# Kernel tuning notes

Measured on AMD Instinct MI355X. Metric: run time of the kernel, lower is better.

## Reference

```python
import math
import jax, jax.numpy as jnp
import numpy as np

COLORS = 10
MAX_SHIFT = 5
B, H, W = 32, 128, 128

_shifts = [(dy, dx) for dy in range(-MAX_SHIFT, MAX_SHIFT + 1)
           for dx in range(-MAX_SHIFT, MAX_SHIFT + 1)
           if not (dy == 0 and dx == 0)]  # include_identity=False
DYS = jnp.asarray(np.array([s[0] for s in _shifts], dtype=np.int32))
DXS = jnp.asarray(np.array([s[1] for s in _shifts], dtype=np.int32))


def _shift_all(grid):
    """Apply every (dy,dx) shift to an int grid [B,H,W] with zero padding.

    out[s, b, y, x] = grid[b, y-dy_s, x-dx_s] if in-bounds else 0,
    exactly matching apply_shift_batch (uncovered regions are color 0).
    Returns [S, B, H, W].
    """
    b, h, w = grid.shape
    padded = jnp.pad(grid, ((0, 0), (MAX_SHIFT, MAX_SHIFT), (MAX_SHIFT, MAX_SHIFT)))
    def one(dy, dx):
        return jax.lax.dynamic_slice(padded, (0, MAX_SHIFT - dy, MAX_SHIFT - dx), (b, h, w))
    return jax.vmap(one)(DYS, DXS)


def setup_inputs() -> dict:
    key = jax.random.key(0)
    k1, k2, k3 = jax.random.split(key, 3)
    return {
        "demo_in": jax.random.randint(k1, (B, H, W), 0, COLORS, dtype=jnp.int32),
        "demo_out": jax.random.randint(k2, (B, H, W), 0, COLORS, dtype=jnp.int32),
        "query_in": jax.random.randint(k3, (B, H, W), 0, COLORS, dtype=jnp.int32),
        "color_log_weight": jnp.zeros((COLORS,), dtype=jnp.float32),
        "logit_scale": jnp.asarray(4.0, dtype=jnp.float32),
    }


def reference(demo_in, demo_out, query_in, color_log_weight, logit_scale):
    b, h, w = query_in.shape
    S = DYS.shape[0]

    # Per-shift correlation score. one_hot(shifted)*one_hot(demo_out)*w summed
    # over (C,H,W) == sum over pixels of w[demo_out] * (shifted == demo_out).
    shifted_demo = _shift_all(demo_in)                       # [S,B,H,W] int
    w_out = jnp.exp(color_log_weight)[demo_out]              # [B,H,W]
    eq = (shifted_demo == demo_out[None]).astype(jnp.float32)
    match = jnp.sum(eq * w_out[None], axis=(2, 3))           # [S,B]
    scale = jnp.minimum(jnp.exp(logit_scale), 100.0)
    scores = match.T / math.sqrt(h * w) * scale              # [B,S]
    attention = jax.nn.softmax(scores, axis=1)               # [B,S]

    # Weighted accumulation of one-hot shifted queries, done as a scatter-add
    # into the color channel (avoids materializing [S,B,C,H,W]).
    shifted_query = _shift_all(query_in)                     # [S,B,H,W] int
    b_idx = jnp.arange(b)[None, :, None, None]
    y_idx = jnp.arange(h)[None, None, :, None]
    x_idx = jnp.arange(w)[None, None, None, :]
    attn_b = jnp.broadcast_to(attention.T[:, :, None, None], (S, b, h, w))
    accum = jnp.zeros((b, COLORS, h, w), dtype=jnp.float32)
    accum = accum.at[b_idx, shifted_query, y_idx, x_idx].add(attn_b)
    return jnp.log(jnp.maximum(accum, 1e-6))
```

## Files before the change

### kernel.cpp

```cpp
#include <hip/hip_runtime.h>
#include <hip/hip_bf16.h>
#include <math.h>

#define COLORS 10
#define NB 32
#define H 128
#define W 128
#define NS 120
#define HW (H*W)
#define STRIPS 8
#define SH 16
#define DROWS 26
#define DINW 8

typedef unsigned char u8;
typedef unsigned int u32;
typedef unsigned long long u64;
typedef float f32x4 __attribute__((ext_vector_type(4)));
typedef short bf16x8 __attribute__((ext_vector_type(8)));

__global__ __launch_bounds__(512) void match_strip(
    const int* __restrict__ demo_in, const int* __restrict__ demo_out,
    const float* __restrict__ clw, float* __restrict__ mpart)
{
    __shared__ u32 din_p[COLORS][DROWS][DINW];
    __shared__ u32 dout_p[COLORS][SH][4];
    __shared__ float wexp[COLORS];

    int t = threadIdx.x;
    int strip = blockIdx.x;
    int b = blockIdx.y;
    int wave = t >> 6, lane = t & 63;

    if (t < COLORS) wexp[t] = __expf(clw[t]);

    const int* di = demo_in  + b * HW;
    const int* dd = demo_out + b * HW;
    int y0 = strip * SH;

    for (int r = wave; r < DROWS; r += 8) {
        int gy = y0 - 5 + r;
        bool ok = (gy >= 0 && gy < H);
        int v0 = 0, v1 = 0;
        if (ok) { v0 = di[gy * W + lane]; v1 = di[gy * W + 64 + lane]; }
        #pragma unroll
        for (int c = 0; c < COLORS; c++) {
            u64 h0 = __ballot(v0 == c);
            u64 h1 = __ballot(v1 == c);
            u64 P0, P1, P2;
            if (!ok) {
                P0 = (c == 0) ? ~0ull : 0ull;
                P1 = P0;
                P2 = (c == 0) ? 0x3FFull : 0ull;
            } else {
                u64 lm = (c == 0) ? 0x1Full  : 0ull;
                u64 rm = (c == 0) ? 0x3E0ull : 0ull;
                P0 = (h0 << 5) | lm;
                P1 = (h0 >> 59) | (h1 << 5);
                P2 = (h1 >> 59) | rm;
            }
            if (lane == 0) {
                u32* w = &din_p[c][r][0];
                w[0] = (u32)P0; w[1] = (u32)(P0 >> 32);
                w[2] = (u32)P1; w[3] = (u32)(P1 >> 32);
                w[4] = (u32)P2; w[5] = 0; w[6] = 0; w[7] = 0;
            }
        }
    }
    for (int r = wave; r < SH; r += 8) {
        int gy = y0 + r;
        int v0 = dd[gy * W + lane], v1 = dd[gy * W + 64 + lane];
        #pragma unroll
        for (int c = 0; c < COLORS; c++) {
            u64 h0 = __ballot(v0 == c);
            u64 h1 = __ballot(v1 == c);
            if (lane == 0) {
                u32* w = &dout_p[c][r][0];
                w[0] = (u32)h0; w[1] = (u32)(h0 >> 32);
                w[2] = (u32)h1; w[3] = (u32)(h1 >> 32);
            }
        }
    }
    __syncthreads();

    int s = t >> 2, q = t & 3;
    float acc = 0.f;
    if (t < 4 * NS) {
        int lin = s + (s >= 60);
        int dy = lin / 11 - 5, dx = lin % 11 - 5;
        int k = 5 - dx;
        for (int c = 0; c < COLORS; c++) {
            int cnt = 0;
            #pragma unroll
            for (int yy = 0; yy < 4; yy++) {
                int y = q * 4 + yy;
                int r = y - dy + 5;
                const u32* dr   = &din_p[c][r][0];
                const u32* orow = &dout_p[c][y][0];
                u32 s0 = __builtin_amdgcn_alignbit(dr[1], dr[0], k);
                u32 s1 = __builtin_amdgcn_alignbit(dr[2], dr[1], k);
                u32 s2 = __builtin_amdgcn_alignbit(dr[3], dr[2], k);
                u32 s3 = __builtin_amdgcn_alignbit(dr[4], dr[3], k);
                cnt += __popc(s0 & orow[0]) + __popc(s1 & orow[1])
                     + __popc(s2 & orow[2]) + __popc(s3 & orow[3]);
            }
            acc += wexp[c] * (float)cnt;
        }
    }
    acc += __shfl_down(acc, 1, 64);
    acc += __shfl_down(acc, 2, 64);
    if (q == 0 && t < 4 * NS)
        mpart[(b * NS + s) * STRIPS + strip] = acc;
}

#define AR 18
__global__ __launch_bounds__(512) void accum_fused(
    const int* __restrict__ query_in, const float* __restrict__ mpart,
    const float* __restrict__ logit_scale, float* __restrict__ out)
{
    __shared__ u8  qs[AR][144];
    __shared__ float sm[NS];
    __shared__ unsigned short abf[128];
    __shared__ __align__(16) u32 Agl[11][64][4];

    int t  = threadIdx.x;
    int y0 = blockIdx.x * 8;
    int b  = blockIdx.y;
    const int* q = query_in + b * HW;

    u32 pk0 = 0, pk1 = 0;
    {
        int g = t;
        #pragma unroll
        for (int e = 0; e < 4; e++) {
            int idx = g * 4 + e;
            int r = idx / 144, p = idx - r * 144;
            int gy = y0 - 5 + r;
            bool ok = (gy >= 0) & (gy < H) & (p >= 5) & (p < 133);
            int cy = gy < 0 ? 0 : (gy > 127 ? 127 : gy);
            int cx = p < 5 ? 0 : (p > 132 ? 127 : p - 5);
            int v = q[cy * W + cx];
            pk0 |= (u32)(ok ? v : 0) << (8 * e);
        }
    }
    if (t < 648 - 512) {
        int g = t + 512;
        #pragma unroll
        for (int e = 0; e < 4; e++) {
            int idx = g * 4 + e;
            int r = idx / 144, p = idx - r * 144;
            int gy = y0 - 5 + r;
            bool ok = (gy >= 0) & (gy < H) & (p >= 5) & (p < 133);
            int cy = gy < 0 ? 0 : (gy > 127 ? 127 : gy);
            int cx = p < 5 ? 0 : (p > 132 ? 127 : p - 5);
            int v = q[cy * W + cx];
            pk1 |= (u32)(ok ? v : 0) << (8 * e);
        }
    }

    float scale = fminf(__expf(logit_scale[0]), 100.0f) * (1.0f / 128.0f);
    if (t < NS) {
        const float* mp = mpart + (t + b * NS) * STRIPS;
        float4 v0 = *reinterpret_cast<const float4*>(mp);
        float4 v1 = *reinterpret_cast<const float4*>(mp + 4);
        sm[t] = (v0.x + v0.y + v0.z + v0.w + v1.x + v1.y + v1.z + v1.w) * scale;
    }

    ((u32*)qs)[t] = pk0;
    if (t < 648 - 512) ((u32*)qs)[t + 512] = pk1;
    __syncthreads();

    if (t < 64) {
        float s0 = sm[t];
        float s1 = (t + 64 < NS) ? sm[t + 64] : -INFINITY;
        float m = fmaxf(s0, s1);
        for (int off = 32; off > 0; off >>= 1) m = fmaxf(m, __shfl_xor(m, off, 64));
        float e0 = __expf(s0 - m);
        float e1 = (t + 64 < NS) ? __expf(s1 - m) : 0.f;
        float sum = e0 + e1;
        for (int off = 32; off > 0; off >>= 1) sum += __shfl_xor(sum, off, 64);
        float inv = 1.0f / sum;
        sm[t] = e0 * inv;
        if (t + 64 < NS) sm[t + 64] = e1 * inv;
    }
    __syncthreads();
    if (t < 128) {
        unsigned short v = 0;
        if (t < 121 && t != 60) {
            int si = t - (t > 60);
            __hip_bfloat16 hb = __float2bfloat16(sm[si]);
            v = *reinterpret_cast<unsigned short*>(&hb);
        }
        abf[t] = v;
    }
    __syncthreads();

    {
        int e = t;
        int st = e >> 6, l = e & 63;
        int mrow = l & 15, g8 = (l >> 4) * 8;
        #pragma unroll
        for (int p = 0; p < 4; p++) {
            int j0 = mrow + 10 - (g8 + p * 2);
            int j1 = j0 - 1;
            int i0 = (j0 >= 0 && j0 <= 10) ? (10 - st) * 11 + j0 : 121;
            int i1 = (j1 >= 0 && j1 <= 10) ? (10 - st) * 11 + j1 : 121;
            Agl[st][l][p] = (u32)abf[i0] | ((u32)abf[i1] << 16);
        }
    }
    if (t < 704 - 512) {
        int e = t + 512;
        int st = e >> 6, l = e & 63;
        int mrow = l & 15, g8 = (l >> 4) * 8;
        #pragma unroll
        for (int p = 0; p < 4; p++) {
            int j0 = mrow + 10 - (g8 + p * 2);
            int j1 = j0 - 1;
            int i0 = (j0 >= 0 && j0 <= 10) ? (10 - st) * 11 + j0 : 121;
            int i1 = (j1 >= 0 && j1 <= 10) ? (10 - st) * 11 + j1 : 121;
            Agl[st][l][p] = (u32)abf[i0] | ((u32)abf[i1] << 16);
        }
    }
    __syncthreads();

    int lane = t & 63, w = t >> 6;
    uint4 afr[11];
    #pragma unroll
    for (int st = 0; st < 11; st++)
        afr[st] = *reinterpret_cast<const uint4*>(&Agl[st][lane][0]);

    int jb = (w >> 2) * 4;
    int xq = w & 3;
    int c = lane & 15, g = lane >> 4;

    #pragma unroll
    for (int ti = 0; ti < 2; ti++) {
        int x0 = xq * 32 + ti * 16;

        uint4 bf[14];
        #pragma unroll
        for (int r = 0; r < 14; r++) {
            u64 eight = *reinterpret_cast<const u64*>(&qs[jb + r][x0 + 8 * g]);
            u32 lo = (u32)eight, hi = (u32)(eight >> 32);
            u32 b0 = ((int)(lo & 255) == c ? 0x3F80u : 0u)
                   | ((int)((lo >> 8)  & 255) == c ? 0x3F800000u : 0u);
            u32 b1 = ((int)((lo >> 16) & 255) == c ? 0x3F80u : 0u)
                   | ((int)((lo >> 24) & 255) == c ? 0x3F800000u : 0u);
            u32 b2 = ((int)(hi & 255) == c ? 0x3F80u : 0u)
                   | ((int)((hi >> 8)  & 255) == c ? 0x3F800000u : 0u);
            u32 b3 = ((int)((hi >> 16) & 255) == c ? 0x3F80u : 0u)
                   | ((int)((hi >> 24) & 255) == c ? 0x3F800000u : 0u);
            bf[r] = make_uint4(b0, b1, b2, b3);
        }

        f32x4 acc[4];
        #pragma unroll
        for (int j = 0; j < 4; j++) acc[j] = (f32x4){0.f, 0.f, 0.f, 0.f};

        #pragma unroll
        for (int st = 0; st < 11; st++) {
            #pragma unroll
            for (int j = 0; j < 4; j++) {
                union { uint4 u; bf16x8 v; } A, B;
                A.u = afr[st];
                B.u = bf[st + j];
                acc[j] = __builtin_amdgcn_mfma_f32_16x16x32_bf16(A.v, B.v, acc[j], 0, 0, 0);
            }
        }

        if (c < COLORS) {
            #pragma unroll
            for (int j = 0; j < 4; j++) {
                float* ob = out + (((size_t)b * COLORS + c) * H + (y0 + jb + j)) * W + x0 + 4 * g;
                float4 rr;
                rr.x = __logf(fmaxf(acc[j][0], 1e-6f));
                rr.y = __logf(fmaxf(acc[j][1], 1e-6f));
                rr.z = __logf(fmaxf(acc[j][2], 1e-6f));
                rr.w = __logf(fmaxf(acc[j][3], 1e-6f));
                *reinterpret_cast<float4*>(ob) = rr;
            }
        }
    }
}

__global__ __launch_bounds__(256) void match_kernel(
    const int* __restrict__ demo_in, const int* __restrict__ demo_out,
    const float* __restrict__ clw, float* __restrict__ match)
{
    int blk = blockIdx.x;
    int b = blk / NS;
    int s = blk % NS;
    int lin = s + (s >= 60 ? 1 : 0);
    int dy = lin / 11 - 5, dx = lin % 11 - 5;

    __shared__ float wexp[COLORS];
    int tid = threadIdx.x;
    if (tid < COLORS) wexp[tid] = expf(clw[tid]);
    __syncthreads();

    const int* __restrict__ din  = demo_in  + b * HW;
    const int* __restrict__ dout = demo_out + b * HW;

    float partial = 0.f;
    for (int i = tid; i < HW; i += 256) {
        int yy = i >> 7, xx = i & 127;
        int co = dout[i];
        int sy = yy - dy, sx = xx - dx;
        int v = 0;
        if (sy >= 0 && sy < H && sx >= 0 && sx < W) v = din[sy * W + sx];
        if (v == co) partial += wexp[co];
    }
    for (int off = 32; off > 0; off >>= 1) partial += __shfl_down(partial, off, 64);
    __shared__ float wsum[4];
    if ((tid & 63) == 0) wsum[tid >> 6] = partial;
    __syncthreads();
    if (tid == 0) match[blk] = wsum[0] + wsum[1] + wsum[2] + wsum[3];
}

__global__ __launch_bounds__(64) void softmax_kernel(
    const float* __restrict__ match, const float* __restrict__ logit_scale,
    float* __restrict__ attention)
{
    int b = blockIdx.x;
    int lane = threadIdx.x;
    float scale = fminf(expf(logit_scale[0]), 100.0f) / sqrtf((float)HW);
    int i0 = lane, i1 = lane + 64;
    float s0 = match[b * NS + i0] * scale;
    float s1 = (i1 < NS) ? match[b * NS + i1] * scale : -INFINITY;
    float m = fmaxf(s0, s1);
    for (int off = 32; off > 0; off >>= 1) m = fmaxf(m, __shfl_xor(m, off, 64));
    float e0 = expf(s0 - m);
    float e1 = (i1 < NS) ? expf(s1 - m) : 0.f;
    float sum = e0 + e1;
    for (int off = 32; off > 0; off >>= 1) sum += __shfl_xor(sum, off, 64);
    float inv = 1.0f / sum;
    attention[b * NS + i0] = e0 * inv;
    if (i1 < NS) attention[b * NS + i1] = e1 * inv;
}

__global__ __launch_bounds__(128) void accum_kernel(
    const int* __restrict__ query_in, const float* __restrict__ attention,
    float* __restrict__ out)
{
    int blk = blockIdx.x;
    int b = blk >> 7;
    int y = blk & 127;
    int x = threadIdx.x;

    __shared__ float att[NS];
    if (threadIdx.x < NS) att[threadIdx.x] = attention[b * NS + threadIdx.x];
    __syncthreads();

    const int* __restrict__ q = query_in + b * HW;
    float acc[COLORS];
    #pragma unroll
    for (int c = 0; c < COLORS; c++) acc[c] = 0.f;

    #pragma unroll 4
    for (int s = 0; s < NS; s++) {
        int lin = s + (s >= 60 ? 1 : 0);
        int dy = lin / 11 - 5, dx = lin % 11 - 5;
        int sy = y - dy, sx = x - dx;
        int v = 0;
        if (sy >= 0 && sy < H && sx >= 0 && sx < W) v = q[sy * W + sx];
        float a = att[s];
        #pragma unroll
        for (int c = 0; c < COLORS; c++) acc[c] += (v == c) ? a : 0.f;
    }
    float* __restrict__ ob = out + (size_t)b * COLORS * HW + y * W + x;
    #pragma unroll
    for (int c = 0; c < COLORS; c++) ob[c * HW] = __logf(fmaxf(acc[c], 1e-6f));
}

extern "C" void kernel_launch(void* const* d_in, const int* in_sizes, int n_in,
                              void* d_out, int out_size, void* d_ws, size_t ws_size,
                              hipStream_t stream) {
    const int*   demo_in     = (const int*)d_in[0];
    const int*   demo_out    = (const int*)d_in[1];
    const int*   query_in    = (const int*)d_in[2];
    const float* clw         = (const float*)d_in[3];
    const float* logit_scale = (const float*)d_in[4];
    float* out = (float*)d_out;

    size_t needed = (size_t)NB * NS * STRIPS * sizeof(float);

    if (ws_size >= needed) {
        float* mpart = (float*)d_ws;
        match_strip<<<dim3(STRIPS, NB), 512, 0, stream>>>(demo_in, demo_out, clw, mpart);
        accum_fused<<<dim3(H / 8, NB), 512, 0, stream>>>(query_in, mpart, logit_scale, out);
    } else {
        float* match = (float*)d_ws;
        float* att   = match + NB * NS;
        match_kernel<<<NB * NS, 256, 0, stream>>>(demo_in, demo_out, clw, match);
        softmax_kernel<<<NB, 64, 0, stream>>>(match, logit_scale, att);
        accum_kernel<<<NB * H, 128, 0, stream>>>(query_in, att, out);
    }
}
```

Before: 29.82 us.

## Restructure MFMA accumulate to 8-row tiles with rolling B-fragment ring buffer

The output kernel changes its wave-to-tile mapping. Each wave now owns a 16-column stripe covering 8 output rows as two 4-row accumulator sets, instead of two 16-column tiles of 4 rows each. B fragments come from a rolling 8-entry ring, built one row per step, and A fragments are loaded from shared memory per step rather than all held in registers. This cuts redundant one-hot B construction and register pressure. Separately, the match kernel widens the packed demo rows to 12 words and uses 16-byte aligned vector shared stores instead of scalar writes.

```diff
diff --git a/kernel.cpp b/kernel.cpp
--- a/kernel.cpp
+++ b/kernel.cpp
@@ -11,7 +11,7 @@
 #define STRIPS 8
 #define SH 16
 #define DROWS 26
-#define DINW 8
+#define DINW 12
 
 typedef unsigned char u8;
 typedef unsigned int u32;
@@ -23,8 +23,8 @@
     const int* __restrict__ demo_in, const int* __restrict__ demo_out,
     const float* __restrict__ clw, float* __restrict__ mpart)
 {
-    __shared__ u32 din_p[COLORS][DROWS][DINW];
-    __shared__ u32 dout_p[COLORS][SH][4];
+    __shared__ __align__(16) u32 din_p[COLORS][DROWS][DINW];
+    __shared__ __align__(16) u32 dout_p[COLORS][SH][4];
     __shared__ float wexp[COLORS];
 
     int t = threadIdx.x;
@@ -60,10 +60,10 @@
                 P2 = (h1 >> 59) | rm;
             }
             if (lane == 0) {
-                u32* w = &din_p[c][r][0];
-                w[0] = (u32)P0; w[1] = (u32)(P0 >> 32);
-                w[2] = (u32)P1; w[3] = (u32)(P1 >> 32);
-                w[4] = (u32)P2; w[5] = 0; w[6] = 0; w[7] = 0;
+                *reinterpret_cast<uint4*>(&din_p[c][r][0]) =
+                    make_uint4((u32)P0, (u32)(P0 >> 32), (u32)P1, (u32)(P1 >> 32));
+                *reinterpret_cast<uint4*>(&din_p[c][r][4]) =
+                    make_uint4((u32)P2, 0u, 0u, 0u);
             }
         }
     }
@@ -74,11 +74,9 @@
         for (int c = 0; c < COLORS; c++) {
             u64 h0 = __ballot(v0 == c);
             u64 h1 = __ballot(v1 == c);
-            if (lane == 0) {
-                u32* w = &dout_p[c][r][0];
-                w[0] = (u32)h0; w[1] = (u32)(h0 >> 32);
-                w[2] = (u32)h1; w[3] = (u32)(h1 >> 32);
-            }
+            if (lane == 0)
+                *reinterpret_cast<uint4*>(&dout_p[c][r][0]) =
+                    make_uint4((u32)h0, (u32)(h0 >> 32), (u32)h1, (u32)(h1 >> 32));
         }
     }
     __syncthreads();
@@ -224,61 +222,63 @@
     __syncthreads();
 
     int lane = t & 63, w = t >> 6;
-    uint4 afr[11];
-    #pragma unroll
-    for (int st = 0; st < 11; st++)
-        afr[st] = *reinterpret_cast<const uint4*>(&Agl[st][lane][0]);
-
-    int jb = (w >> 2) * 4;
-    int xq = w & 3;
+    int x0 = w * 16;
     int c = lane & 15, g = lane >> 4;
 
-    #pragma unroll
-    for (int ti = 0; ti < 2; ti++) {
-        int x0 = xq * 32 + ti * 16;
-
-        uint4 bf[14];
-        #pragma unroll
-        for (int r = 0; r < 14; r++) {
-            u64 eight = *reinterpret_cast<const u64*>(&qs[jb + r][x0 + 8 * g]);
-            u32 lo = (u32)eight, hi = (u32)(eight >> 32);
-            u32 b0 = ((int)(lo & 255) == c ? 0x3F80u : 0u)
-                   | ((int)((lo >> 8)  & 255) == c ? 0x3F800000u : 0u);
-            u32 b1 = ((int)((lo >> 16) & 255) == c ? 0x3F80u : 0u)
-                   | ((int)((lo >> 24) & 255) == c ? 0x3F800000u : 0u);
-            u32 b2 = ((int)(hi & 255) == c ? 0x3F80u : 0u)
-                   | ((int)((hi >> 8)  & 255) == c ? 0x3F800000u : 0u);
-            u32 b3 = ((int)((hi >> 16) & 255) == c ? 0x3F80u : 0u)
-                   | ((int)((hi >> 24) & 255) == c ? 0x3F800000u : 0u);
-            bf[r] = make_uint4(b0, b1, b2, b3);
-        }
-
-        f32x4 acc[4];
-        #pragma unroll
-        for (int j = 0; j < 4; j++) acc[j] = (f32x4){0.f, 0.f, 0.f, 0.f};
-
-        #pragma unroll
-        for (int st = 0; st < 11; st++) {
-            #pragma unroll
-            for (int j = 0; j < 4; j++) {
-                union { uint4 u; bf16x8 v; } A, B;
-                A.u = afr[st];
-                B.u = bf[st + j];
-                acc[j] = __builtin_amdgcn_mfma_f32_16x16x32_bf16(A.v, B.v, acc[j], 0, 0, 0);
-            }
-        }
-
-        if (c < COLORS) {
-            #pragma unroll
-            for (int j = 0; j < 4; j++) {
-                float* ob = out + (((size_t)b * COLORS + c) * H + (y0 + jb + j)) * W + x0 + 4 * g;
-                float4 rr;
-                rr.x = __logf(fmaxf(acc[j][0], 1e-6f));
-                rr.y = __logf(fmaxf(acc[j][1], 1e-6f));
-                rr.z = __logf(fmaxf(acc[j][2], 1e-6f));
-                rr.w = __logf(fmaxf(acc[j][3], 1e-6f));
-                *reinterpret_cast<float4*>(ob) = rr;
-            }
+    #define BUILD_B(r) ({                                                        \
+        u64 eight = *reinterpret_cast<const u64*>(&qs[(r)][x0 + 8 * g]);         \
+        u32 lo = (u32)eight, hi = (u32)(eight >> 32);                            \
+        u32 b0 = ((int)(lo & 255) == c ? 0x3F80u : 0u)                           \
+               | ((int)((lo >> 8)  & 255) == c ? 0x3F800000u : 0u);              \
+        u32 b1 = ((int)((lo >> 16) & 255) == c ? 0x3F80u : 0u)                   \
+               | ((int)((lo >> 24) & 255) == c ? 0x3F800000u : 0u);              \
+        u32 b2 = ((int)(hi & 255) == c ? 0x3F80u : 0u)                           \
+               | ((int)((hi >> 8)  & 255) == c ? 0x3F800000u : 0u);              \
+        u32 b3 = ((int)((hi >> 16) & 255) == c ? 0x3F80u : 0u)                   \
+               | ((int)((hi >> 24) & 255) == c ? 0x3F800000u : 0u);              \
+        make_uint4(b0, b1, b2, b3); })
+
+    uint4 bf[8];
+    #pragma unroll
+    for (int r = 0; r < 7; r++) bf[r & 7] = BUILD_B(r);
+
+    f32x4 acc0[4], acc1[4];
+    #pragma unroll
+    for (int j = 0; j < 4; j++) { acc0[j] = (f32x4){0,0,0,0}; acc1[j] = (f32x4){0,0,0,0}; }
+
+    #pragma unroll
+    for (int st = 0; st < 11; st++) {
+        bf[(st + 7) & 7] = BUILD_B(st + 7);
+        uint4 a4 = *reinterpret_cast<const uint4*>(&Agl[st][lane][0]);
+        union { uint4 u; bf16x8 v; } A; A.u = a4;
+        #pragma unroll
+        for (int j = 0; j < 4; j++) {
+            union { uint4 u; bf16x8 v; } B0, B1;
+            B0.u = bf[(st + j) & 7];
+            B1.u = bf[(st + 4 + j) & 7];
+            acc0[j] = __builtin_amdgcn_mfma_f32_16x16x32_bf16(A.v, B0.v, acc0[j], 0, 0, 0);
+            acc1[j] = __builtin_amdgcn_mfma_f32_16x16x32_bf16(A.v, B1.v, acc1[j], 0, 0, 0);
+        }
+    }
+    #undef BUILD_B
+
+    if (c < COLORS) {
+        #pragma unroll
+        for (int j = 0; j < 4; j++) {
+            float* ob0 = out + (((size_t)b * COLORS + c) * H + (y0 + j)) * W + x0 + 4 * g;
+            float4 r0;
+            r0.x = __logf(fmaxf(acc0[j][0], 1e-6f));
+            r0.y = __logf(fmaxf(acc0[j][1], 1e-6f));
+            r0.z = __logf(fmaxf(acc0[j][2], 1e-6f));
+            r0.w = __logf(fmaxf(acc0[j][3], 1e-6f));
+            *reinterpret_cast<float4*>(ob0) = r0;
+            float* ob1 = out + (((size_t)b * COLORS + c) * H + (y0 + 4 + j)) * W + x0 + 4 * g;
+            float4 r1;
+            r1.x = __logf(fmaxf(acc1[j][0], 1e-6f));
+            r1.y = __logf(fmaxf(acc1[j][1], 1e-6f));
+            r1.z = __logf(fmaxf(acc1[j][2], 1e-6f));
+            r1.w = __logf(fmaxf(acc1[j][3], 1e-6f));
+            *reinterpret_cast<float4*>(ob1) = r1;
         }
     }
 }
```

After: 28.65 us. -3.9%, faster.
